# Kernel tuning notes

Hardware: AMD Instinct MI355X
Metric: run time of the kernel (lower is better)

The kernel has to match this reference:

```python
import jax, jax.numpy as jnp
import numpy as np

B, S, HID = 2, 2048, 2048
H, KH, D = 16, 4, 128  # heads, kv heads, head_dim
N_REP = H // KH
SCALE = D ** -0.5


def rotate_half(x):
    x1, x2 = x[..., : D // 2], x[..., D // 2:]
    return jnp.concatenate((-x2, x1), axis=-1)


def setup_inputs() -> dict:
    key = jax.random.key(0)
    ks = jax.random.split(key, 6)
    hidden_states = jax.random.normal(ks[0], (B, S, HID), jnp.float32)
    # standard RoPE cos/sin tables, shape [B, S, D]
    inv_freq = 1.0 / (10000.0 ** (np.arange(0, D, 2, dtype=np.float32) / D))
    pos = np.arange(S, dtype=np.float32)
    freqs = np.outer(pos, inv_freq)            # [S, D/2]
    emb = np.concatenate([freqs, freqs], -1)   # [S, D]
    cos = jnp.broadcast_to(jnp.cos(emb), (B, S, D)).astype(jnp.float32)
    sin = jnp.broadcast_to(jnp.sin(emb), (B, S, D)).astype(jnp.float32)
    # additive causal mask [1, 1, S, S]
    neg = jnp.finfo(jnp.float32).min
    causal = jnp.triu(jnp.full((S, S), neg, jnp.float32), k=1)
    attention_mask = causal[None, None]
    std = 0.02
    wq = jax.random.normal(ks[1], (HID, H * D), jnp.float32) * std
    wk = jax.random.normal(ks[2], (HID, KH * D), jnp.float32) * std
    wv = jax.random.normal(ks[3], (HID, KH * D), jnp.float32) * std
    wo = jax.random.normal(ks[4], (H * D, HID), jnp.float32) * std
    return {"hidden_states": hidden_states, "cos": cos, "sin": sin,
            "attention_mask": attention_mask, "wq": wq, "wk": wk, "wv": wv, "wo": wo}


def reference(hidden_states, cos, sin, attention_mask, wq, wk, wv, wo):
    b, s, _ = hidden_states.shape
    q = (hidden_states @ wq).reshape(b, s, H, D).transpose(0, 2, 1, 3)   # [b,H,s,d]
    k = (hidden_states @ wk).reshape(b, s, KH, D).transpose(0, 2, 1, 3)  # [b,KH,s,d]
    v = (hidden_states @ wv).reshape(b, s, KH, D).transpose(0, 2, 1, 3)
    c = cos[:, None, :, :]  # [b,1,s,d] broadcast over heads
    sn = sin[:, None, :, :]
    q = q * c + rotate_half(q) * sn
    k = k * c + rotate_half(k) * sn
    # GQA: repeat KV heads
    k = jnp.repeat(k, N_REP, axis=1)  # [b,H,s,d]
    v = jnp.repeat(v, N_REP, axis=1)
    scores = jnp.einsum('bhqd,bhkd->bhqk', q, k) * SCALE + attention_mask
    probs = jax.nn.softmax(scores, axis=-1)
    attn = jnp.einsum('bhqk,bhkd->bhqd', probs, v)
    attn = attn.transpose(0, 2, 1, 3).reshape(b, s, H * D)
    return attn @ wo
```

## Files before the change

kernel.cpp:

```cpp
#include <hip/hip_runtime.h>
#include <stdint.h>

#define Bc   2
#define Sc   2048
#define HIDc 2048
#define Hc   16
#define KHc  4
#define Dc   128
#define HDc  2048
#define KHDc 512
#define QKVS 3072
#define SCALE2c 0.12751744657f
#define M0c 6.0f
#define N_ITEMS 1536

typedef _Float16 f16;
typedef _Float16 f16x2 __attribute__((ext_vector_type(2)));
typedef _Float16 f16x4 __attribute__((ext_vector_type(4)));
typedef _Float16 f16x8 __attribute__((ext_vector_type(8)));
typedef float    f32x4 __attribute__((ext_vector_type(4)));

__device__ __forceinline__ void gl_lds16(const void* g, void* l) {
  __builtin_amdgcn_global_load_lds(
      (const __attribute__((address_space(1))) unsigned int*)g,
      (__attribute__((address_space(3))) unsigned int*)l, 16, 0, 0);
}

__global__ __launch_bounds__(256) void conv_hs(const float* __restrict__ in,
                                               f16* __restrict__ out,
                                               int* __restrict__ ctr) {
  if (blockIdx.x == 0 && threadIdx.x == 0) *ctr = 0;
  int i = (blockIdx.x * 256 + threadIdx.x) * 4;
  float4 v = *(const float4*)&in[i];
  f16x4 o; o[0] = (f16)v.x; o[1] = (f16)v.y; o[2] = (f16)v.z; o[3] = (f16)v.w;
  *(f16x4*)&out[i] = o;
}

__global__ __launch_bounds__(256) void trw_all(const float* __restrict__ wq,
                                               const float* __restrict__ wk,
                                               const float* __restrict__ wv,
                                               const float* __restrict__ wo,
                                               f16* __restrict__ wqkvT,
                                               f16* __restrict__ woT) {
  const int z = blockIdx.z;
  const float* in; f16* out; int C, rowOff;
  if (z == 0)      { in = wq; out = wqkvT; C = 2048; rowOff = 0; }
  else if (z == 1) { in = wk; out = wqkvT; C = 512;  rowOff = 2048; }
  else if (z == 2) { in = wv; out = wqkvT; C = 512;  rowOff = 2560; }
  else             { in = wo; out = woT;   C = 2048; rowOff = 0; }
  if (blockIdx.x * 64 >= C) return;
  __shared__ float Ld[64 * 65];
  const int tid = threadIdx.x;
  const int r0 = blockIdx.y * 64, c0 = blockIdx.x * 64;
#pragma unroll
  for (int p = 0; p < 4; ++p) {
    int idx = p * 256 + tid;
    int r = idx >> 4, c4 = (idx & 15) * 4;
    float4 v = *(const float4*)&in[(size_t)(r0 + r) * C + c0 + c4];
    Ld[r * 65 + c4 + 0] = v.x; Ld[r * 65 + c4 + 1] = v.y;
    Ld[r * 65 + c4 + 2] = v.z; Ld[r * 65 + c4 + 3] = v.w;
  }
  __syncthreads();
#pragma unroll
  for (int p = 0; p < 4; ++p) {
    int idx = p * 256 + tid;
    int oc = idx >> 4, m4 = (idx & 15) * 4;
    f16x4 o;
#pragma unroll
    for (int i = 0; i < 4; ++i) o[i] = (f16)Ld[(m4 + i) * 65 + oc];
    *(f16x4*)&out[(size_t)(rowOff + c0 + oc) * 2048 + r0 + m4] = o;
  }
}

__global__ __launch_bounds__(256) void rope_all(f16* __restrict__ x,
                                                const float* __restrict__ cb,
                                                const float* __restrict__ sb) {
  int bid = blockIdx.x;
  int colbase, log2h, idx;
  if (bid < 16384) { colbase = 0;    log2h = 4; idx = bid * 256 + threadIdx.x; }
  else             { colbase = 2048; log2h = 2; idx = (bid - 16384) * 256 + threadIdx.x; }
  int d   = idx & 63;
  int h   = (idx >> 6) & ((1 << log2h) - 1);
  int row = idx >> (6 + log2h);
  f16* p = x + (size_t)row * QKVS + colbase + h * 128;
  float x1 = (float)p[d], x2 = (float)p[64 + d];
  float c = cb[(size_t)row * 128 + d], s = sb[(size_t)row * 128 + d];
  p[d]      = (f16)(x1 * c - x2 * s);
  p[64 + d] = (f16)(x2 * c + x1 * s);
}

__global__ __launch_bounds__(256) void v_tr(const f16* __restrict__ QKV,
                                            f16* __restrict__ Vt) {
  __shared__ f16 Ld[64 * 78];
  const int tid = threadIdx.x;
  const int s0 = blockIdx.x * 64, d0 = blockIdx.y * 64;
  const int b = blockIdx.z >> 2, kh = blockIdx.z & 3;
#pragma unroll
  for (int p = 0; p < 2; ++p) {
    int idx = p * 256 + tid;
    int sl = idx >> 3, dc8 = (idx & 7) * 8;
    f16x8 v = *(const f16x8*)&QKV[(size_t)(b * Sc + s0 + sl) * QKVS + 2560 + kh * 128 + d0 + dc8];
#pragma unroll
    for (int i = 0; i < 4; ++i) {
      f16x2 w; w[0] = v[2 * i]; w[1] = v[2 * i + 1];
      *(f16x2*)&Ld[sl * 78 + dc8 + 2 * i] = w;
    }
  }
  __syncthreads();
  {
    int dr = (tid >> 3) * 2, sc8 = (tid & 7) * 8;
    f16x8 r0v, r1v;
#pragma unroll
    for (int j = 0; j < 8; ++j) {
      f16x2 w = *(const f16x2*)&Ld[(sc8 + j) * 78 + dr];
      r0v[j] = w[0]; r1v[j] = w[1];
    }
    size_t obase = ((size_t)(b * KHc + kh) * 128 + d0 + dr) * Sc + s0 + sc8;
    *(f16x8*)&Vt[obase]      = r0v;
    *(f16x8*)&Vt[obase + Sc] = r1v;
  }
}

__global__ __launch_bounds__(256) void gemm_bt(const f16* __restrict__ A,
                                               const f16* __restrict__ Bt,
                                               void* __restrict__ Cout,
                                               int M, int N, int K, int c_f16) {
  __shared__ f16 Al[128 * 64];
  __shared__ f16 Bl[128 * 64];
  const int tid  = threadIdx.x;
  const int lane = tid & 63, wave = tid >> 6;
  const int quad = lane >> 4, l16 = lane & 15;
  const int wm = (wave >> 1) * 64, wn = (wave & 1) * 64;
  const int m0 = blockIdx.y * 128, n0 = blockIdx.x * 128;
  f32x4 acc[4][4] = {};

  for (int k0 = 0; k0 < K; k0 += 64) {
    __syncthreads();
#pragma unroll
    for (int p = 0; p < 4; ++p) {
      const int g  = wave * 2 + (p >> 1);
      const int kq = (p & 1) * 4 + quad;
      gl_lds16(&A [(size_t)(m0 + g * 16 + l16) * K + k0 + kq * 8], &Al[(wave * 4 + p) * 512]);
      gl_lds16(&Bt[(size_t)(n0 + g * 16 + l16) * K + k0 + kq * 8], &Bl[(wave * 4 + p) * 512]);
    }
    __syncthreads();
#pragma unroll
    for (int ks = 0; ks < 2; ++ks) {
      f16x8 af[4], bf[4];
#pragma unroll
      for (int i = 0; i < 4; ++i)
        af[i] = *(const f16x8*)&Al[((((wave >> 1) * 4 + i) * 8 + ks * 4 + quad) * 16 + l16) * 8];
#pragma unroll
      for (int j = 0; j < 4; ++j)
        bf[j] = *(const f16x8*)&Bl[((((wave & 1) * 4 + j) * 8 + ks * 4 + quad) * 16 + l16) * 8];
#pragma unroll
      for (int i = 0; i < 4; ++i)
#pragma unroll
        for (int j = 0; j < 4; ++j)
          acc[i][j] = __builtin_amdgcn_mfma_f32_16x16x32_f16(af[i], bf[j], acc[i][j], 0, 0, 0);
    }
  }

  if (c_f16) {
    f16* C = (f16*)Cout;
#pragma unroll
    for (int i = 0; i < 4; ++i)
#pragma unroll
      for (int j = 0; j < 4; ++j)
#pragma unroll
        for (int r = 0; r < 4; ++r)
          C[(size_t)(m0 + wm + i * 16 + quad * 4 + r) * N + n0 + wn + j * 16 + l16] =
              (f16)acc[i][j][r];
  } else {
    float* C = (float*)Cout;
#pragma unroll
    for (int i = 0; i < 4; ++i)
#pragma unroll
      for (int j = 0; j < 4; ++j)
#pragma unroll
        for (int r = 0; r < 4; ++r)
          C[(size_t)(m0 + wm + i * 16 + quad * 4 + r) * N + n0 + wn + j * 16 + l16] =
              acc[i][j][r];
  }
}

__global__ __launch_bounds__(256) void gemm_qkv96(const f16* __restrict__ A,
                                                  const f16* __restrict__ Bt,
                                                  f16* __restrict__ C) {
  __shared__ f16 Al[128 * 64];
  __shared__ f16 Bl[96 * 64];
  const int tid  = threadIdx.x;
  const int lane = tid & 63, wave = tid >> 6;
  const int quad = lane >> 4, l16 = lane & 15;
  const int wm = (wave >> 1) * 64;
  const int wnG = (wave & 1) * 3;
  const int m0 = blockIdx.y * 128, n0 = blockIdx.x * 96;
  const int K = 2048;
  f32x4 acc[4][3] = {};

  for (int k0 = 0; k0 < K; k0 += 64) {
    __syncthreads();
#pragma unroll
    for (int p = 0; p < 4; ++p) {
      const int g  = wave * 2 + (p >> 1);
      const int kq = (p & 1) * 4 + quad;
      gl_lds16(&A[(size_t)(m0 + g * 16 + l16) * K + k0 + kq * 8], &Al[(wave * 4 + p) * 512]);
    }
#pragma unroll
    for (int p = 0; p < 3; ++p) {
      const int gb = wave * 3 + p;
      const int gi = gb >> 1, kh2 = gb & 1;
      gl_lds16(&Bt[(size_t)(n0 + gi * 16 + l16) * K + k0 + kh2 * 32 + quad * 8], &Bl[gb * 512]);
    }
    __syncthreads();
#pragma unroll
    for (int ks = 0; ks < 2; ++ks) {
      f16x8 af[4], bf[3];
#pragma unroll
      for (int i = 0; i < 4; ++i)
        af[i] = *(const f16x8*)&Al[((((wave >> 1) * 4 + i) * 8 + ks * 4 + quad) * 16 + l16) * 8];
#pragma unroll
      for (int j = 0; j < 3; ++j)
        bf[j] = *(const f16x8*)&Bl[(((wnG + j) * 8 + ks * 4 + quad) * 16 + l16) * 8];
#pragma unroll
      for (int i = 0; i < 4; ++i)
#pragma unroll
        for (int j = 0; j < 3; ++j)
          acc[i][j] = __builtin_amdgcn_mfma_f32_16x16x32_f16(af[i], bf[j], acc[i][j], 0, 0, 0);
    }
  }

#pragma unroll
  for (int i = 0; i < 4; ++i)
#pragma unroll
    for (int j = 0; j < 3; ++j)
#pragma unroll
      for (int r = 0; r < 4; ++r)
        C[(size_t)(m0 + wm + i * 16 + quad * 4 + r) * QKVS + n0 + (wnG + j) * 16 + l16] =
            (f16)acc[i][j][r];
}

__global__ __launch_bounds__(256, 4) void attn_v6(const f16* __restrict__ QKV,
                                                  const f16* __restrict__ Vt,
                                                  f16* __restrict__ Ob,
                                                  f16* __restrict__ Opart,
                                                  float2* __restrict__ ML,
                                                  int* __restrict__ ctr) {
  __shared__ f16 Kl[64 * 128];
  __shared__ f16 Vl[64 * 128];
  __shared__ f16 Ps[4 * 512];
  __shared__ int item_s;
  const int tid  = threadIdx.x;
  const int lane = tid & 63, wave = tid >> 6;
  const int quad = lane >> 4, l16 = lane & 15;

  f16x8 ones_f;
#pragma unroll
  for (int i = 0; i < 8; ++i) ones_f[i] = (l16 == 0) ? (f16)1.0f : (f16)0.0f;

  for (;;) {
    if (tid == 0) item_s = atomicAdd(ctr, 1);
    __syncthreads();
    const int item = item_s;
    if (item >= N_ITEMS) break;

    int qt, bh, k0t, k1t, hf = -1;
    if (item < 1280) {
      int base = 0, c = 32;
#pragma unroll 1
      for (; c >= 17; --c) {
        int sz = (c & 1) ? 64 : 96;
        if (item < base + sz) break;
        base += sz;
      }
      int off = item - base;
      if (off < 64) {
        qt = c - 1; hf = off >> 5; bh = off & 31;
        int nk = qt + 1, hn = nk >> 1;
        k0t = hf ? hn : 0; k1t = hf ? nk : hn;
      } else {
        qt = (c >> 1) - 1; bh = off - 64; k0t = 0; k1t = qt + 1;
      }
    } else {
      int off = item - 1280;
      qt = 7 - (off >> 5); bh = off & 31; k0t = 0; k1t = qt + 1;
    }
    const int b = bh >> 4, h = bh & 15, kh = h >> 2;
    const int qbase = qt * 64 + wave * 16;

    f16x8 qf[4];
    {
      const f16* qp = QKV + (size_t)(b * Sc + qbase + l16) * QKVS + h * 128 + quad * 8;
#pragma unroll
      for (int c = 0; c < 4; ++c) qf[c] = *(const f16x8*)(qp + c * 32);
    }
    f32x4 ls = {};
    f32x4 o[8] = {};

    auto stageK = [&](int kt) {
#pragma unroll
      for (int p = 0; p < 4; ++p)
        gl_lds16(&QKV[(size_t)(b * Sc + kt * 64 + wave * 16 + l16) * QKVS + 2048 + kh * 128 + p * 32 + quad * 8],
                 &Kl[(wave * 4 + p) * 512]);
    };
    auto stageV = [&](int kt) {
#pragma unroll
      for (int p = 0; p < 4; ++p) {
        const int dt = wave * 2 + (p >> 1), kc = p & 1;
        gl_lds16(&Vt[(size_t)((b * KHc + kh) * 128 + dt * 16 + l16) * Sc + kt * 64 + kc * 32 + quad * 8],
                 &Vl[(wave * 4 + p) * 512]);
      }
    };

    stageK(k0t);
    stageV(k0t);

    for (int kt = k0t; kt < k1t; ++kt) {
      const bool more = (kt + 1 < k1t);

      asm volatile("s_waitcnt vmcnt(4)" ::: "memory");
      __builtin_amdgcn_sched_barrier(0);
      __builtin_amdgcn_s_barrier();
      __builtin_amdgcn_sched_barrier(0);

      __builtin_amdgcn_s_setprio(1);
      f32x4 s4[4] = {};
#pragma unroll
      for (int kc = 0; kc < 2; ++kc)
#pragma unroll
        for (int c = 0; c < 4; ++c) {
          f16x8 ka = *(const f16x8*)&Kl[(((kc * 2 + 0) * 4 + c) * 4 + quad) * 128 + l16 * 8];
          f16x8 kb = *(const f16x8*)&Kl[(((kc * 2 + 1) * 4 + c) * 4 + quad) * 128 + l16 * 8];
          s4[kc * 2 + 0] = __builtin_amdgcn_mfma_f32_16x16x32_f16(qf[c], ka, s4[kc * 2 + 0], 0, 0, 0);
          s4[kc * 2 + 1] = __builtin_amdgcn_mfma_f32_16x16x32_f16(qf[c], kb, s4[kc * 2 + 1], 0, 0, 0);
        }
      __builtin_amdgcn_s_setprio(0);

      __builtin_amdgcn_sched_barrier(0);
      __builtin_amdgcn_s_barrier();
      __builtin_amdgcn_sched_barrier(0);
      if (more) stageK(kt + 1);

      const bool diag = (kt == qt);
      const int cb = kt * 64 + l16;
      const int wb  = wave * 512 + (l16 & 7);
      const int rhi = l16 >> 3;
      float e2[4], e3[4];
#pragma unroll
      for (int r = 0; r < 4; ++r) {
        float v0 = fmaf(s4[0][r], SCALE2c, -M0c);
        float v1 = fmaf(s4[1][r], SCALE2c, -M0c);
        float v2 = fmaf(s4[2][r], SCALE2c, -M0c);
        float v3 = fmaf(s4[3][r], SCALE2c, -M0c);
        if (diag) {
          const int qrow = qbase + quad * 4 + r;
          if (cb      > qrow) v0 = -1e30f;
          if (cb + 16 > qrow) v1 = -1e30f;
          if (cb + 32 > qrow) v2 = -1e30f;
          if (cb + 48 > qrow) v3 = -1e30f;
        }
        float p0 = exp2f(v0), p1 = exp2f(v1);
        e2[r] = exp2f(v2); e3[r] = exp2f(v3);
        const int rowoff = (quad * 4 + r) * 8;
        Ps[wb + (rhi + 0) * 128 + rowoff] = (f16)p0;
        Ps[wb + (rhi + 2) * 128 + rowoff] = (f16)p1;
      }

      if (more) { asm volatile("s_waitcnt vmcnt(4)" ::: "memory"); }
      else      { asm volatile("s_waitcnt vmcnt(0)" ::: "memory"); }
      __builtin_amdgcn_sched_barrier(0);
      __builtin_amdgcn_s_barrier();
      __builtin_amdgcn_sched_barrier(0);

      {
        f16x8 pf = *(const f16x8*)&Ps[wave * 512 + quad * 128 + l16 * 8];
        __builtin_amdgcn_s_setprio(1);
        ls = __builtin_amdgcn_mfma_f32_16x16x32_f16(pf, ones_f, ls, 0, 0, 0);
#pragma unroll
        for (int dt = 0; dt < 8; ++dt) {
          f16x8 vf = *(const f16x8*)&Vl[((dt * 2 + 0) * 4 + quad) * 128 + l16 * 8];
          o[dt] = __builtin_amdgcn_mfma_f32_16x16x32_f16(pf, vf, o[dt], 0, 0, 0);
        }
        __builtin_amdgcn_s_setprio(0);
      }
#pragma unroll
      for (int r = 0; r < 4; ++r) {
        const int rowoff = (quad * 4 + r) * 8;
        Ps[wb + (rhi + 0) * 128 + rowoff] = (f16)e2[r];
        Ps[wb + (rhi + 2) * 128 + rowoff] = (f16)e3[r];
      }
      {
        f16x8 pf = *(const f16x8*)&Ps[wave * 512 + quad * 128 + l16 * 8];
        __builtin_amdgcn_s_setprio(1);
        ls = __builtin_amdgcn_mfma_f32_16x16x32_f16(pf, ones_f, ls, 0, 0, 0);
#pragma unroll
        for (int dt = 0; dt < 8; ++dt) {
          f16x8 vf = *(const f16x8*)&Vl[((dt * 2 + 1) * 4 + quad) * 128 + l16 * 8];
          o[dt] = __builtin_amdgcn_mfma_f32_16x16x32_f16(pf, vf, o[dt], 0, 0, 0);
        }
        __builtin_amdgcn_s_setprio(0);
      }

      __builtin_amdgcn_sched_barrier(0);
      __builtin_amdgcn_s_barrier();
      __builtin_amdgcn_sched_barrier(0);
      if (more) stageV(kt + 1);
    }

    float inv[4], lrow[4];
#pragma unroll
    for (int r = 0; r < 4; ++r) {
      lrow[r] = __shfl(ls[r], lane & 48);
      inv[r] = 1.0f / lrow[r];
    }
    if (hf < 0) {
#pragma unroll
      for (int dt = 0; dt < 8; ++dt)
#pragma unroll
        for (int r = 0; r < 4; ++r)
          Ob[(size_t)(b * Sc + qbase + quad * 4 + r) * HDc + h * 128 + dt * 16 + l16] =
              (f16)(o[dt][r] * inv[r]);
    } else {
      const int tile = (qt - 16) * 32 + bh;
      f16* op = Opart + ((size_t)tile * 2 + hf) * (64 * 128);
#pragma unroll
      for (int dt = 0; dt < 8; ++dt)
#pragma unroll
        for (int r = 0; r < 4; ++r)
          op[(wave * 16 + quad * 4 + r) * 128 + dt * 16 + l16] = (f16)(o[dt][r] * inv[r]);
      if (l16 == 0) {
#pragma unroll
        for (int r = 0; r < 4; ++r) {
          float2 ml; ml.x = M0c; ml.y = lrow[r];
          ML[((size_t)tile * 2 + hf) * 64 + wave * 16 + quad * 4 + r] = ml;
        }
      }
    }
  }
}

__global__ __launch_bounds__(256) void attn_merge(const f16* __restrict__ Opart,
                                                  const float2* __restrict__ ML,
                                                  f16* __restrict__ Ob) {
  const int tile = blockIdx.x;
  const int qt = 16 + (tile >> 5), bh = tile & 31;
  const int b = bh >> 4, h = bh & 15;
  const int tid = threadIdx.x;
  const int row = tid >> 2, c0 = (tid & 3) * 32;
  float2 ml1 = ML[(size_t)tile * 2 * 64 + row];
  float2 ml2 = ML[((size_t)tile * 2 + 1) * 64 + row];
  float m = fmaxf(ml1.x, ml2.x);
  float w1 = ml1.y * exp2f(ml1.x - m);
  float w2 = ml2.y * exp2f(ml2.x - m);
  float rinv = 1.0f / (w1 + w2);
  float a1 = w1 * rinv, a2 = w2 * rinv;
  const f16* o1 = Opart + (size_t)tile * 2 * (64 * 128) + row * 128 + c0;
  const f16* o2 = o1 + 64 * 128;
  f16* out = Ob + (size_t)(b * Sc + qt * 64 + row) * HDc + h * 128 + c0;
#pragma unroll
  for (int j = 0; j < 4; ++j) {
    f16x8 x1 = *(const f16x8*)(o1 + j * 8);
    f16x8 x2 = *(const f16x8*)(o2 + j * 8);
    f16x8 y;
#pragma unroll
    for (int i = 0; i < 8; ++i) y[i] = (f16)(a1 * (float)x1[i] + a2 * (float)x2[i]);
    *(f16x8*)(out + j * 8) = y;
  }
}

extern "C" void kernel_launch(void* const* d_in, const int* in_sizes, int n_in,
                              void* d_out, int out_size, void* d_ws, size_t ws_size,
                              hipStream_t stream) {
  (void)in_sizes; (void)n_in; (void)out_size; (void)ws_size;
  const float* hs   = (const float*)d_in[0];
  const float* cosb = (const float*)d_in[1];
  const float* sinb = (const float*)d_in[2];
  const float* wq = (const float*)d_in[4];
  const float* wk = (const float*)d_in[5];
  const float* wv = (const float*)d_in[6];
  const float* wo = (const float*)d_in[7];
  float* out = (float*)d_out;

  char* ws = (char*)d_ws;
  int*  ctr = (int*)ws;
  size_t off = 256;
  auto alloc = [&](size_t bytes) { char* p = ws + off; off += (bytes + 255) & ~(size_t)255; return p; };
  f16*  hsF   = (f16*)alloc((size_t)Bc * Sc * HIDc * 2);
  f16*  woT   = (f16*)alloc((size_t)HIDc * HDc * 2);
  f16*  QKVf  = (f16*)alloc((size_t)Bc * Sc * QKVS * 2);
  f16*  Vt_g  = (f16*)alloc((size_t)Bc * KHc * Dc * Sc * 2);
  f16*  wqkvT = (f16*)alloc((size_t)QKVS * HIDc * 2);
  f16*  Opart = wqkvT;
  {
    size_t opart_bytes = (size_t)512 * 2 * 64 * 128 * 2;
    size_t wqkvT_bytes = (size_t)QKVS * HIDc * 2;
    if (opart_bytes > wqkvT_bytes) off += opart_bytes - wqkvT_bytes;
  }
  float2* ML = (float2*)alloc((size_t)512 * 2 * 64 * sizeof(float2));
  f16*  attnF = hsF;

  conv_hs<<<8192, 256, 0, stream>>>(hs, hsF, ctr);
  trw_all<<<dim3(32, 32, 4), 256, 0, stream>>>(wq, wk, wv, wo, wqkvT, woT);

  gemm_qkv96<<<dim3(32, 32), 256, 0, stream>>>(hsF, wqkvT, QKVf);

  rope_all<<<20480, 256, 0, stream>>>(QKVf, cosb, sinb);
  v_tr<<<dim3(32, 2, 8), 256, 0, stream>>>(QKVf, Vt_g);

  attn_v6<<<1024, 256, 0, stream>>>(QKVf, Vt_g, attnF, Opart, ML, ctr);
  attn_merge<<<512, 256, 0, stream>>>(Opart, ML, attnF);

  gemm_bt<<<dim3(16, 32), 256, 0, stream>>>(attnF, woT, out, 4096, 2048, 2048, 0);
}
```

Before: 430.1 us.

## Replace projection GEMMs with double-buffered 512-thread templated GEMM

Both the QKV and output projection GEMMs now use one templated kernel with 512 threads and 256-row tiles. It double-buffers the LDS tiles so the next K-slice loads while MFMAs run, keeps per-wave B fragments in registers, and raises wave priority around the MFMA bursts. This should hide global-to-LDS latency and cut barrier count per MFMA, at the cost of larger LDS use and more registers per thread. The output GEMM now uses 128-wide N tiles and the QKV GEMM 192-wide, which reduces the block count.

```diff
diff --git a/kernel.cpp b/kernel.cpp
--- a/kernel.cpp
+++ b/kernel.cpp
@@ -121,123 +121,83 @@
   }
 }
 
-__global__ __launch_bounds__(256) void gemm_bt(const f16* __restrict__ A,
-                                               const f16* __restrict__ Bt,
-                                               void* __restrict__ Cout,
-                                               int M, int N, int K, int c_f16) {
-  __shared__ f16 Al[128 * 64];
-  __shared__ f16 Bl[128 * 64];
+template<int NREP, int CF16>
+__global__ __launch_bounds__(512, 2) void gemm8p(const f16* __restrict__ A,
+                                                 const f16* __restrict__ Bt,
+                                                 void* __restrict__ Cout,
+                                                 int K, int cstride) {
+  __shared__ f16 Al[2][16384];
+  __shared__ f16 Bl[2][NREP * 4096];
   const int tid  = threadIdx.x;
   const int lane = tid & 63, wave = tid >> 6;
   const int quad = lane >> 4, l16 = lane & 15;
-  const int wm = (wave >> 1) * 64, wn = (wave & 1) * 64;
-  const int m0 = blockIdx.y * 128, n0 = blockIdx.x * 128;
-  f32x4 acc[4][4] = {};
-
-  for (int k0 = 0; k0 < K; k0 += 64) {
-    __syncthreads();
+  const int wm = wave >> 2, wn = wave & 3;
+  const int m0 = blockIdx.y * 256, n0 = blockIdx.x * (NREP * 64);
+  f32x4 acc[8][NREP] = {};
+
+  auto stage = [&](int buf, int k0) {
 #pragma unroll
     for (int p = 0; p < 4; ++p) {
       const int g  = wave * 2 + (p >> 1);
       const int kq = (p & 1) * 4 + quad;
-      gl_lds16(&A [(size_t)(m0 + g * 16 + l16) * K + k0 + kq * 8], &Al[(wave * 4 + p) * 512]);
-      gl_lds16(&Bt[(size_t)(n0 + g * 16 + l16) * K + k0 + kq * 8], &Bl[(wave * 4 + p) * 512]);
-    }
+      gl_lds16(&A[(size_t)(m0 + g * 16 + l16) * K + k0 + kq * 8],
+               &Al[buf][(wave * 4 + p) * 512]);
+    }
+#pragma unroll
+    for (int p = 0; p < NREP; ++p) {
+      const int gb = wave * NREP + p;
+      const int gi = gb >> 1, kh2 = gb & 1;
+      gl_lds16(&Bt[(size_t)(n0 + gi * 16 + l16) * K + k0 + kh2 * 32 + quad * 8],
+               &Bl[buf][gb * 512]);
+    }
+  };
+
+  stage(0, 0);
+  const int NT = K >> 6;
+  for (int t = 0; t < NT; ++t) {
+    const int cur = t & 1;
     __syncthreads();
-#pragma unroll
-    for (int ks = 0; ks < 2; ++ks) {
-      f16x8 af[4], bf[4];
+    if (t + 1 < NT) stage(cur ^ 1, (t + 1) * 64);
+
+    f16x8 bf[NREP][2];
+#pragma unroll
+    for (int j = 0; j < NREP; ++j)
+#pragma unroll
+      for (int ks = 0; ks < 2; ++ks)
+        bf[j][ks] = *(const f16x8*)&Bl[cur][(((wn * NREP + j) * 8 + ks * 4 + quad) * 16 + l16) * 8];
+#pragma unroll
+    for (int mh = 0; mh < 2; ++mh) {
+      f16x8 af[4][2];
 #pragma unroll
       for (int i = 0; i < 4; ++i)
-        af[i] = *(const f16x8*)&Al[((((wave >> 1) * 4 + i) * 8 + ks * 4 + quad) * 16 + l16) * 8];
-#pragma unroll
-      for (int j = 0; j < 4; ++j)
-        bf[j] = *(const f16x8*)&Bl[((((wave & 1) * 4 + j) * 8 + ks * 4 + quad) * 16 + l16) * 8];
-#pragma unroll
-      for (int i = 0; i < 4; ++i)
-#pragma unroll
-        for (int j = 0; j < 4; ++j)
-          acc[i][j] = __builtin_amdgcn_mfma_f32_16x16x32_f16(af[i], bf[j], acc[i][j], 0, 0, 0);
-    }
-  }
-
-  if (c_f16) {
-    f16* C = (f16*)Cout;
-#pragma unroll
-    for (int i = 0; i < 4; ++i)
-#pragma unroll
-      for (int j = 0; j < 4; ++j)
-#pragma unroll
-        for (int r = 0; r < 4; ++r)
-          C[(size_t)(m0 + wm + i * 16 + quad * 4 + r) * N + n0 + wn + j * 16 + l16] =
-              (f16)acc[i][j][r];
-  } else {
-    float* C = (float*)Cout;
-#pragma unroll
-    for (int i = 0; i < 4; ++i)
-#pragma unroll
-      for (int j = 0; j < 4; ++j)
-#pragma unroll
-        for (int r = 0; r < 4; ++r)
-          C[(size_t)(m0 + wm + i * 16 + quad * 4 + r) * N + n0 + wn + j * 16 + l16] =
-              acc[i][j][r];
-  }
-}
-
-__global__ __launch_bounds__(256) void gemm_qkv96(const f16* __restrict__ A,
-                                                  const f16* __restrict__ Bt,
-                                                  f16* __restrict__ C) {
-  __shared__ f16 Al[128 * 64];
-  __shared__ f16 Bl[96 * 64];
-  const int tid  = threadIdx.x;
-  const int lane = tid & 63, wave = tid >> 6;
-  const int quad = lane >> 4, l16 = lane & 15;
-  const int wm = (wave >> 1) * 64;
-  const int wnG = (wave & 1) * 3;
-  const int m0 = blockIdx.y * 128, n0 = blockIdx.x * 96;
-  const int K = 2048;
-  f32x4 acc[4][3] = {};
-
-  for (int k0 = 0; k0 < K; k0 += 64) {
-    __syncthreads();
-#pragma unroll
-    for (int p = 0; p < 4; ++p) {
-      const int g  = wave * 2 + (p >> 1);
-      const int kq = (p & 1) * 4 + quad;
-      gl_lds16(&A[(size_t)(m0 + g * 16 + l16) * K + k0 + kq * 8], &Al[(wave * 4 + p) * 512]);
-    }
-#pragma unroll
-    for (int p = 0; p < 3; ++p) {
-      const int gb = wave * 3 + p;
-      const int gi = gb >> 1, kh2 = gb & 1;
-      gl_lds16(&Bt[(size_t)(n0 + gi * 16 + l16) * K + k0 + kh2 * 32 + quad * 8], &Bl[gb * 512]);
-    }
-    __syncthreads();
-#pragma unroll
-    for (int ks = 0; ks < 2; ++ks) {
-      f16x8 af[4], bf[3];
-#pragma unroll
-      for (int i = 0; i < 4; ++i)
-        af[i] = *(const f16x8*)&Al[((((wave >> 1) * 4 + i) * 8 + ks * 4 + quad) * 16 + l16) * 8];
-#pragma unroll
-      for (int j = 0; j < 3; ++j)
-        bf[j] = *(const f16x8*)&Bl[(((wnG + j) * 8 + ks * 4 + quad) * 16 + l16) * 8];
-#pragma unroll
-      for (int i = 0; i < 4; ++i)
-#pragma unroll
-        for (int j = 0; j < 3; ++j)
-          acc[i][j] = __builtin_amdgcn_mfma_f32_16x16x32_f16(af[i], bf[j], acc[i][j], 0, 0, 0);
-    }
-  }
-
-#pragma unroll
-  for (int i = 0; i < 4; ++i)
-#pragma unroll
-    for (int j = 0; j < 3; ++j)
-#pragma unroll
-      for (int r = 0; r < 4; ++r)
-        C[(size_t)(m0 + wm + i * 16 + quad * 4 + r) * QKVS + n0 + (wnG + j) * 16 + l16] =
-            (f16)acc[i][j][r];
+#pragma unroll
+        for (int ks = 0; ks < 2; ++ks)
+          af[i][ks] = *(const f16x8*)&Al[cur][(((wm * 8 + mh * 4 + i) * 8 + ks * 4 + quad) * 16 + l16) * 8];
+      __builtin_amdgcn_s_setprio(1);
+#pragma unroll
+      for (int ks = 0; ks < 2; ++ks)
+#pragma unroll
+        for (int i = 0; i < 4; ++i)
+#pragma unroll
+          for (int j = 0; j < NREP; ++j)
+            acc[mh * 4 + i][j] = __builtin_amdgcn_mfma_f32_16x16x32_f16(
+                af[i][ks], bf[j][ks], acc[mh * 4 + i][j], 0, 0, 0);
+      __builtin_amdgcn_s_setprio(0);
+    }
+  }
+
+  const int rbase = m0 + wm * 128;
+  const int cbase = n0 + wn * NREP * 16;
+#pragma unroll
+  for (int mi = 0; mi < 8; ++mi)
+#pragma unroll
+    for (int j = 0; j < NREP; ++j)
+#pragma unroll
+      for (int r = 0; r < 4; ++r) {
+        size_t idx = (size_t)(rbase + mi * 16 + quad * 4 + r) * cstride + cbase + j * 16 + l16;
+        if (CF16) ((f16*)Cout)[idx]   = (f16)acc[mi][j][r];
+        else      ((float*)Cout)[idx] = acc[mi][j][r];
+      }
 }
 
 __global__ __launch_bounds__(256, 4) void attn_v6(const f16* __restrict__ QKV,
@@ -502,7 +462,7 @@
   conv_hs<<<8192, 256, 0, stream>>>(hs, hsF, ctr);
   trw_all<<<dim3(32, 32, 4), 256, 0, stream>>>(wq, wk, wv, wo, wqkvT, woT);
 
-  gemm_qkv96<<<dim3(32, 32), 256, 0, stream>>>(hsF, wqkvT, QKVf);
+  gemm8p<3, 1><<<dim3(16, 16), 512, 0, stream>>>(hsF, wqkvT, QKVf, 2048, QKVS);
 
   rope_all<<<20480, 256, 0, stream>>>(QKVf, cosb, sinb);
   v_tr<<<dim3(32, 2, 8), 256, 0, stream>>>(QKVf, Vt_g);
@@ -510,5 +470,5 @@
   attn_v6<<<1024, 256, 0, stream>>>(QKVf, Vt_g, attnF, Opart, ML, ctr);
   attn_merge<<<512, 256, 0, stream>>>(Opart, ML, attnF);
 
-  gemm_bt<<<dim3(16, 32), 256, 0, stream>>>(attnF, woT, out, 4096, 2048, 2048, 0);
-}
+  gemm8p<2, 0><<<dim3(16, 16), 512, 0, stream>>>(attnF, woT, out, 2048, 2048);
+}
```

After: 411.3 us. 1.05x faster.
